# Kernel tuning notes

Measured on AMD Instinct MI355X. Metric: run time of the kernel, lower is better.

## Reference

```python
import jax, jax.numpy as jnp
from jax import lax
import numpy as np

B, S, IN = 8, 4096, 64
D, H, K = 512, 8, 3
TCN_CH = [256, 256, 512]
HD = D // H


def setup_inputs() -> dict:
    key = jax.random.key(0)
    ks = iter(jax.random.split(key, 64))
    def nrm(shape, s=0.02):
        return jax.random.normal(next(ks), shape, jnp.float32) * s
    inp = {"x": jax.random.normal(next(ks), (B, S, IN), jnp.float32)}
    inp["W_in"] = nrm((IN, D)); inp["b_in"] = jnp.zeros((D,), jnp.float32)
    chans = [D] + TCN_CH
    for i in range(3):
        cin, cout = chans[i], chans[i + 1]
        inp[f"c1w{i}"] = nrm((cout, cin, K), 0.01); inp[f"c1b{i}"] = jnp.zeros((cout,), jnp.float32)
        inp[f"c2w{i}"] = nrm((cout, cout, K), 0.01); inp[f"c2b{i}"] = jnp.zeros((cout,), jnp.float32)
        if cin != cout:  # downsample 1x1 conv (blocks 0 and 2)
            inp[f"dsw{i}"] = nrm((cout, cin, 1), 0.01); inp[f"dsb{i}"] = jnp.zeros((cout,), jnp.float32)
    inp["W_tcn"] = nrm((TCN_CH[-1], D)); inp["b_tcn"] = jnp.zeros((D,), jnp.float32)
    NL = 2  # attention layers, stacked on leading axis
    for n in ["Wq", "Wk", "Wv", "Wo"]:
        inp[n] = nrm((NL, D, D))
    for n in ["bq", "bk", "bv", "bo", "ln_b"]:
        inp[n] = jnp.zeros((NL, D), jnp.float32)
    inp["ln_g"] = jnp.ones((NL, D), jnp.float32)
    inp["W_out"] = nrm((D, 1)); inp["b_out"] = jnp.zeros((1,), jnp.float32)
    return inp


def _conv(x, w, b, dil, pad):
    # x: (B,C,L), w: (O,I,K)
    y = lax.conv_general_dilated(x, w, (1,), [(pad, pad)], rhs_dilation=(dil,),
                                 dimension_numbers=("NCH", "OIH", "NCH"))
    return y + b[None, :, None]


def _block(t, c1w, c1b, c2w, c2b, ds, dil):
    # TemporalConvBlock: symmetric padding (k-1)*dil on both convs, truncate to input length
    pad = (K - 1) * dil
    o = jax.nn.relu(_conv(t, c1w, c1b, dil, pad))   # length L + pad
    o = _conv(o, c2w, c2b, dil, pad)                # length L + 2*pad
    r = t if ds is None else _conv(t, ds[0], ds[1], 1, 0)
    return jax.nn.relu(o[:, :, : t.shape[2]] + r)


def _layernorm(x, g, b, eps=1e-5):
    mu = x.mean(-1, keepdims=True)
    var = ((x - mu) ** 2).mean(-1, keepdims=True)
    return (x - mu) * lax.rsqrt(var + eps) * g + b


def _forward(x, W_in, b_in, c1w0, c1b0, c2w0, c2b0, dsw0, dsb0,
             c1w1, c1b1, c2w1, c2b1, c1w2, c1b2, c2w2, c2b2, dsw2, dsb2,
             W_tcn, b_tcn, Wq, bq, Wk, bk, Wv, bv, Wo, bo, ln_g, ln_b, W_out, b_out):
    h = x @ W_in + b_in                              # (B,S,D)
    t = jnp.swapaxes(h, 1, 2)                        # (B,D,S)
    t = _block(t, c1w0, c1b0, c2w0, c2b0, (dsw0, dsb0), 1)
    t = _block(t, c1w1, c1b1, c2w1, c2b1, None, 2)
    t = _block(t, c1w2, c1b2, c2w2, c2b2, (dsw2, dsb2), 4)
    h = h + jnp.swapaxes(t, 1, 2) @ W_tcn + b_tcn
    # sinusoidal positional encoding
    pos = jnp.arange(S, dtype=jnp.float32)[:, None]
    div = jnp.exp(jnp.arange(0, D, 2, dtype=jnp.float32) * (-np.log(10000.0) / D))
    pe = jnp.stack([jnp.sin(pos * div), jnp.cos(pos * div)], axis=-1).reshape(S, D)
    h = h + pe[None]
    for l in range(Wq.shape[0]):
        res = h
        def heads(y):  # (B,S,D) -> (B,H,S,HD)
            return y.reshape(B, S, H, HD).transpose(0, 2, 1, 3)
        q = heads(h @ Wq[l] + bq[l])
        k = heads(h @ Wk[l] + bk[l])
        v = heads(h @ Wv[l] + bv[l])
        qf = jax.nn.elu(q) + 1.0
        kf = jax.nn.elu(k) + 1.0
        kv = jnp.einsum("bhnd,bhnm->bhdm", kf, v)            # (B,H,HD,HD)
        out = jnp.einsum("bhnd,bhdm->bhnm", qf, kv)          # (B,H,S,HD)
        norm = jnp.maximum(jnp.einsum("bhnd,bhd->bhn", qf, kf.sum(2)), 1e-6)
        out = out / norm[..., None]
        out = out.transpose(0, 2, 1, 3).reshape(B, S, D)
        h = _layernorm(res + out @ Wo[l] + bo[l], ln_g[l], ln_b[l])
    pooled = h.mean(1)                                       # (B,D)
    return (pooled @ W_out + b_out)[:, 0]                    # (B,)


def reference(x, W_in, b_in, c1w0, c1b0, c2w0, c2b0, dsw0, dsb0,
              c1w1, c1b1, c2w1, c2b1, c1w2, c1b2, c2w2, c2b2, dsw2, dsb2,
              W_tcn, b_tcn, Wq, bq, Wk, bk, Wv, bv, Wo, bo, ln_g, ln_b, W_out, b_out):
    return _forward(x, W_in, b_in, c1w0, c1b0, c2w0, c2b0, dsw0, dsb0,
                    c1w1, c1b1, c2w1, c2b1, c1w2, c1b2, c2w2, c2b2, dsw2, dsb2,
                    W_tcn, b_tcn, Wq, bq, Wk, bk, Wv, bv, Wo, bo, ln_g, ln_b, W_out, b_out)
```

## Files before the change

### kernel.cpp

```cpp
#include <hip/hip_runtime.h>

typedef unsigned short u16;
typedef unsigned int u32;
typedef short bhalf8 __attribute__((ext_vector_type(8)));
typedef float f32x4 __attribute__((ext_vector_type(4)));

#define S_LEN 4096
#define NSEG 30

__device__ __forceinline__ float b2f(u16 h){ return __uint_as_float(((u32)h) << 16); }
__device__ __forceinline__ u16 f2b(float f){
  u32 u = __float_as_uint(f);
  return (u16)((u + 0x7FFFu + ((u >> 16) & 1u)) >> 16);
}
__device__ __forceinline__ u32 cvtpk(float a, float b){
  u32 r; asm("v_cvt_pk_bf16_f32 %0, %1, %2" : "=v"(r) : "v"(a), "v"(b)); return r;
}
__device__ __forceinline__ void unp8(uint4 v, float* f){
  f[0]=__uint_as_float(v.x<<16); f[1]=__uint_as_float(v.x&0xffff0000u);
  f[2]=__uint_as_float(v.y<<16); f[3]=__uint_as_float(v.y&0xffff0000u);
  f[4]=__uint_as_float(v.z<<16); f[5]=__uint_as_float(v.z&0xffff0000u);
  f[6]=__uint_as_float(v.w<<16); f[7]=__uint_as_float(v.w&0xffff0000u);
}
__device__ __forceinline__ void unp4(uint2 v, float* f){
  f[0]=__uint_as_float(v.x<<16); f[1]=__uint_as_float(v.x&0xffff0000u);
  f[2]=__uint_as_float(v.y<<16); f[3]=__uint_as_float(v.y&0xffff0000u);
}

__device__ __forceinline__ size_t taddr(int r, int c, int C){
  return (size_t)(r >> 7) * ((size_t)C << 7) + (size_t)((c >> 5) << 12)
       + ((r & 127) << 5) + (c & 31);
}

__device__ __forceinline__ void gload16(const void* g, void* l){
  __builtin_amdgcn_global_load_lds(
      (__attribute__((address_space(1))) void*)(g),
      (__attribute__((address_space(3))) void*)(l), 16, 0, 0);
}

struct PrepArgs {
  const float* src[NSEG];
  int N[NSEG]; int K[NSEG]; int sn[NSEG]; int sk[NSEG]; unsigned off[NSEG];
};

__global__ __launch_bounds__(256) void prep_w(PrepArgs pa, u16* __restrict__ wb){
  int seg = blockIdx.y;
  int N = pa.N[seg], K = pa.K[seg];
  int ntk = (K + 31) >> 5;
  int tiles = ((N + 31) >> 5) * ntk;
  int tile = blockIdx.x;
  if (tile >= tiles) return;
  int n0 = (tile / ntk) << 5, k0 = (tile % ntk) << 5;
  const float* src = pa.src[seg];
  long sn = pa.sn[seg], sk = pa.sk[seg];
  u16* dst = wb + pa.off[seg];
  int lk = threadIdx.x & 31, ln = threadIdx.x >> 5;
  #pragma unroll
  for (int i = 0; i < 4; ++i){
    int n = n0 + ln + i*8, k = k0 + lk;
    if (n < N && k < K)
      dst[(size_t)n*K + k] = f2b(src[(long)n*sn + (long)k*sk]);
  }
}

__global__ __launch_bounds__(256) void pe_k(float* __restrict__ pe){
  int id = blockIdx.x*256 + threadIdx.x;
  int s = id >> 8, i = id & 255;
  float div = expf((float)i * (-2.0f * 9.210340371976184f / 512.0f));
  float a = (float)s * div;
  pe[(size_t)s*512 + 2*i]   = sinf(a);
  pe[(size_t)s*512 + 2*i+1] = cosf(a);
}

__global__ __launch_bounds__(256) void cvt_k(const float* __restrict__ x, u16* __restrict__ xb, int n){
  int id = blockIdx.x*256 + threadIdx.x;
  if (id < n){
    int r = id >> 6, c = id & 63;
    xb[taddr(r, c, 64)] = f2b(x[id]);
  }
}

template<int KTOT>
__global__ __launch_bounds__(512, 1) void gemm8_k(
    const u16* __restrict__ A, const u16* __restrict__ W,
    const float* __restrict__ bias, const float* __restrict__ bias2,
    const float* __restrict__ bias3,
    u16* __restrict__ out, const u16* __restrict__ resb,
    const float* __restrict__ peb,
    int N, int nN, int flags)
{
  constexpr int KT = KTOT >> 6;
  constexpr int IT = KT >> 1;
  __shared__ u16 As[2][16384];
  __shared__ u16 Bs[2][16384];
  const int tid = threadIdx.x;
  const int wave = tid >> 6, lane = tid & 63;
  const int wm = wave >> 2, wn = wave & 3;
  const int c0 = lane >> 4, fro = lane & 15;

  const int nwg = gridDim.x;
  const int lin = blockIdx.x;
  const int swz = (lin & 7) * (nwg >> 3) + (lin >> 3);
  const int mb = swz / nN, nb = swz - mb * nN;
  const int m0 = mb << 8, n0 = nb << 8;

  const f32x4 zf = {0.f,0.f,0.f,0.f};
  f32x4 acc[8][4];
  #pragma unroll
  for (int i=0;i<8;++i)
    #pragma unroll
    for (int j=0;j<4;++j) acc[i][j] = zf;

  bhalf8 af[2][2], bf[4][2];

  auto SA = [&](int t, int q){
    int s = (q << 9) + tid;
    int row = s >> 3, phys = s & 7;
    int lc = phys ^ (row & 7);
    int grow = m0 + row;
    int gcol = (t << 6) + (lc << 3);
    size_t ga = ((size_t)(grow >> 7) << 16) + (size_t)((gcol >> 5) << 12)
              + ((grow & 127) << 5) + (gcol & 31);
    gload16(A + ga, &As[t & 1][(q << 12) + (wave << 9)]);
  };
  auto SB = [&](int t, int j){
    int s = (j << 9) + tid;
    int row = s >> 3, phys = s & 7;
    int lc = phys ^ (row & 7);
    gload16(W + (size_t)(n0 + row) * KTOT + (t << 6) + (lc << 3),
            &Bs[t & 1][(j << 12) + (wave << 9)]);
  };
  auto LDB = [&](int t){
    #pragma unroll
    for (int nt=0;nt<4;++nt)
      #pragma unroll
      for (int ks=0;ks<2;++ks){
        int row = (wn << 6) + (nt << 4) + fro;
        int phys = ((ks << 2) + c0) ^ (row & 7);
        bf[nt][ks] = *(const bhalf8*)&Bs[t & 1][(row << 6) + (phys << 3)];
      }
  };
  auto LDA = [&](int t, int q){
    #pragma unroll
    for (int mtl=0;mtl<2;++mtl)
      #pragma unroll
      for (int ks=0;ks<2;++ks){
        int row = (q << 6) + (wm << 5) + (mtl << 4) + fro;
        int phys = ((ks << 2) + c0) ^ (row & 7);
        af[mtl][ks] = *(const bhalf8*)&As[t & 1][(row << 6) + (phys << 3)];
      }
  };
  auto BAR = [&]{
    __builtin_amdgcn_sched_barrier(0);
    __builtin_amdgcn_s_barrier();
    __builtin_amdgcn_sched_barrier(0);
  };
  auto MM = [&](int q){
    __builtin_amdgcn_s_setprio(1);
    #pragma unroll
    for (int mtl=0;mtl<2;++mtl)
      #pragma unroll
      for (int nt=0;nt<4;++nt){
        acc[(q<<1)+mtl][nt] = __builtin_amdgcn_mfma_f32_16x16x32_bf16(
            bf[nt][0], af[mtl][0], acc[(q<<1)+mtl][nt], 0, 0, 0);
        acc[(q<<1)+mtl][nt] = __builtin_amdgcn_mfma_f32_16x16x32_bf16(
            bf[nt][1], af[mtl][1], acc[(q<<1)+mtl][nt], 0, 0, 0);
      }
    __builtin_amdgcn_s_setprio(0);
  };

  #pragma unroll
  for (int x=0;x<4;++x){ SA(0,x); SB(0,x); }
  #pragma unroll
  for (int x=0;x<3;++x){ SA(1,x); SB(1,x); }
  asm volatile("s_waitcnt vmcnt(6)" ::: "memory");
  BAR();

  #pragma unroll
  for (int i=0;i<IT;++i){
    const int t0 = 2*i, t1 = 2*i+1, t2 = 2*i+2, t3 = 2*i+3;
    #pragma unroll
    for (int q=0;q<4;++q){
      if (q == 0) LDB(t0);
      LDA(t0, q);
      if (q == 0){ SA(t1,3); SB(t1,3); }
      else if (t2 < KT){ SA(t2,q-1); SB(t2,q-1); }
      BAR();
      MM(q);
      if (q == 3){
        if (t2 < KT) asm volatile("s_waitcnt vmcnt(6)" ::: "memory");
        else         asm volatile("s_waitcnt vmcnt(0)" ::: "memory");
      }
      BAR();
    }
    #pragma unroll
    for (int q=0;q<4;++q){
      if (q == 0) LDB(t1);
      LDA(t1, q);
      if (q == 0){ if (t2 < KT){ SA(t2,3); SB(t2,3); } }
      else if (t3 < KT){ SA(t3,q-1); SB(t3,q-1); }
      BAR();
      MM(q);
      if (q == 3 && (i + 1 < IT))
        asm volatile("s_waitcnt vmcnt(6)" ::: "memory");
      BAR();
    }
  }

  const int th = n0 >> 9;
  #pragma unroll
  for (int mt = 0; mt < 8; ++mt){
    const int row = m0 + ((mt >> 1) << 6) + (wm << 5) + ((mt & 1) << 4) + fro;
    const size_t prow = (size_t)(row & (S_LEN - 1)) * 512;
    #pragma unroll
    for (int nt = 0; nt < 4; ++nt){
      const int col = n0 + (wn << 6) + (nt << 4) + (c0 << 2);
      float v0 = acc[mt][nt][0], v1 = acc[mt][nt][1], v2 = acc[mt][nt][2], v3 = acc[mt][nt][3];
      if (flags & 32){
        const float* bp = (th == 0) ? bias : ((th == 1) ? bias2 : bias3);
        if (bp){ float4 b4 = *(const float4*)&bp[col & 511]; v0+=b4.x; v1+=b4.y; v2+=b4.z; v3+=b4.w; }
      } else {
        if (bias){ float4 b4 = *(const float4*)&bias[col]; v0+=b4.x; v1+=b4.y; v2+=b4.z; v3+=b4.w; }
      }
      if (flags & 4){
        uint2 rv = *(const uint2*)(resb + taddr(row, col, N));
        float rf[4]; unp4(rv, rf);
        v0 += rf[0]; v1 += rf[1]; v2 += rf[2]; v3 += rf[3];
      }
      if (flags & 8){
        float4 p4 = *(const float4*)&peb[prow + col];
        v0 += p4.x; v1 += p4.y; v2 += p4.z; v3 += p4.w;
      }
      if (flags & 1){
        v0 = fmaxf(v0, 0.f); v1 = fmaxf(v1, 0.f); v2 = fmaxf(v2, 0.f); v3 = fmaxf(v3, 0.f);
      }
      if ((flags & 2) && (!(flags & 32) || th < 2)){
        v0 = (v0 > 0.f) ? (v0 + 1.f) : __expf(v0);
        v1 = (v1 > 0.f) ? (v1 + 1.f) : __expf(v1);
        v2 = (v2 > 0.f) ? (v2 + 1.f) : __expf(v2);
        v3 = (v3 > 0.f) ? (v3 + 1.f) : __expf(v3);
      }
      uint2 pk; pk.x = cvtpk(v0, v1); pk.y = cvtpk(v2, v3);
      *(uint2*)(out + taddr(row, col, N)) = pk;
    }
  }
}

template<int NTAPS, int KS1, int KS2>
__global__ __launch_bounds__(256) void gemm_k(
    const u16* __restrict__ A, const u16* __restrict__ W,
    const u16* __restrict__ A2, const u16* __restrict__ W2,
    const float* __restrict__ bias, const float* __restrict__ bias2,
    const float* __restrict__ bias3,
    u16* __restrict__ out, const u16* __restrict__ resb,
    const float* __restrict__ peb, const float* __restrict__ den,
    int N, int CA, int CA2, int dil, int nN, int wbstride, int flags)
{
  constexpr bool MT   = (NTAPS == 3);
  constexpr int HALO  = MT ? 8 : 0;
  constexpr int AR    = MT ? 144 : 128;
  constexpr int DA    = (!MT) ? 3 : ((KS2 > 0) ? 4 : 2);
  constexpr int DB    = MT ? 4 : 3;
  constexpr int K     = KS1 << 5;
  constexpr int K2    = KS2 << 5;
  constexpr int TOTAL = MT ? (3*KS1 + KS2) : (KS1 + KS2);
  __shared__ u16 As[DA][AR*32];
  __shared__ u16 Bs[DB][128*32];
  const int tid = threadIdx.x;
  const int wave = tid >> 6, lane = tid & 63;
  const int wm = wave >> 1, wn = wave & 1;

  const int nwg = gridDim.x;
  const int lin = blockIdx.x;
  const int swz = (lin & 7) * (nwg >> 3) + (lin >> 3);
  const int mb = swz / nN, nb = swz - mb * nN;
  const int m0 = mb << 7, n0 = nb << 7;
  const bool bnd = (m0 & (S_LEN - 1)) == 0;

  const u16* Ae = (flags & 16) ? (A + (((size_t)(n0 & 511) >> 5) << 12)) : A;

  const int lr4 = lane >> 2, lc4 = lane & 3;
  const int c0 = lane >> 4, fro = lane & 15;

  const f32x4 zf = {0.f, 0.f, 0.f, 0.f};
  const bhalf8 zb = {0,0,0,0,0,0,0,0};
  f32x4 acc[4][4];
  #pragma unroll
  for (int i=0;i<4;++i)
    #pragma unroll
    for (int j=0;j<4;++j) acc[i][j] = zf;

  const u16* Wb = W + (size_t)(m0 >> 12) * (size_t)wbstride;
  const size_t abase  = (size_t)mb * ((size_t)CA  << 7);
  const size_t abase2 = (size_t)mb * ((size_t)CA2 << 7);

  auto STAGE_A = [&](int kb, int ab){
    const size_t tb = abase + ((size_t)kb << 12);
    #pragma unroll
    for (int half = 0; half < 2; ++half){
      int mrow = (wave << 5) + (half << 4) + lr4;
      int i = mrow + HALO;
      int cg = lc4 ^ ((i >> 1) & 3);
      gload16(Ae + tb + mrow*32 + (cg << 3), &As[ab][(HALO + (wave << 5) + (half << 4)) * 32]);
    }
    if (MT && wave == 0 && lane < 32){
      int j = lr4;
      int cg = lc4 ^ ((j >> 1) & 3);
      size_t hb_ = (mb ? abase - ((size_t)CA << 7) : abase) + ((size_t)kb << 12) + (120 + j)*32;
      gload16(Ae + hb_ + (cg << 3), &As[ab][0]);
    }
  };
  auto STAGE_A2 = [&](int t2, int ab){
    const size_t tb = abase2 + ((size_t)t2 << 12);
    #pragma unroll
    for (int half = 0; half < 2; ++half){
      int mrow = (wave << 5) + (half << 4) + lr4;
      int i = mrow + HALO;
      int cg = lc4 ^ ((i >> 1) & 3);
      gload16(A2 + tb + mrow*32 + (cg << 3), &As[ab][(HALO + (wave << 5) + (half << 4)) * 32]);
    }
  };
  auto STAGE_B = [&](const u16* Wt, size_t kstride, int kb, int bb){
    #pragma unroll
    for (int half = 0; half < 2; ++half){
      int i = (wave << 5) + (half << 4) + lr4;
      int cg = lc4 ^ ((i >> 1) & 3);
      gload16(Wt + (size_t)(n0 + i) * kstride + (kb << 5) + (cg << 3),
              &Bs[bb][((wave << 5) + (half << 4)) * 32]);
    }
  };
  auto DO16 = [&](int ab, int bb, int sh, bool mask){
    bhalf8 af[4], bf[4];
    #pragma unroll
    for (int mt = 0; mt < 4; ++mt){
      int r8 = (wm << 6) + (mt << 4) + fro + HALO + sh;
      af[mt] = *(const bhalf8*)&As[ab][r8 * 32 + ((c0 ^ ((r8 >> 1) & 3)) << 3)];
    }
    if (MT && mask && bnd && wm == 0 && fro + sh < 0) af[0] = zb;
    #pragma unroll
    for (int nt = 0; nt < 4; ++nt){
      int rB = (wn << 6) + (nt << 4) + fro;
      bf[nt] = *(const bhalf8*)&Bs[bb][rB * 32 + ((c0 ^ ((rB >> 1) & 3)) << 3)];
    }
    #pragma unroll
    for (int mt = 0; mt < 4; ++mt)
      #pragma unroll
      for (int nt = 0; nt < 4; ++nt)
        acc[mt][nt] = __builtin_amdgcn_mfma_f32_16x16x32_bf16(bf[nt], af[mt], acc[mt][nt], 0, 0, 0);
  };

  if constexpr (!MT){
    auto STG = [&](int s){
      int b = s % 3;
      if (s < KS1){ STAGE_A(s, b); STAGE_B(Wb, (size_t)K, s, b); }
      else if (KS2 > 0){ STAGE_A2(s - KS1, b); STAGE_B(W2, (size_t)K2, s - KS1, b); }
    };
    STG(0);
    if constexpr (TOTAL > 1) STG(1);
    #pragma unroll
    for (int s = 0; s < TOTAL; ++s){
      if (s + 1 >= TOTAL) asm volatile("s_waitcnt vmcnt(0)" ::: "memory");
      else                asm volatile("s_waitcnt vmcnt(4)" ::: "memory");
      __builtin_amdgcn_sched_barrier(0);
      __builtin_amdgcn_s_barrier();
      __builtin_amdgcn_sched_barrier(0);
      if (s + 2 < TOTAL) STG(s + 2);
      DO16(s % 3, s % 3, 0, false);
    }
  } else {
    auto STG = [&](int s){
      if (s < 3*KS1){
        int kb = s / 3, tap = s % 3;
        if (tap == 0) STAGE_A(kb, kb & (DA-1));
        STAGE_B(Wb + (size_t)tap * N * K, (size_t)K, kb, s & 3);
      } else if (KS2 > 0){
        int t2 = s - 3*KS1;
        STAGE_A2(t2, (KS1 + t2) & (DA-1));
        STAGE_B(W2, (size_t)K2, t2, s & 3);
      }
    };
    STG(0);
    if constexpr (TOTAL > 1) STG(1);
    if constexpr (TOTAL > 2) STG(2);
    #pragma unroll
    for (int s = 0; s < TOTAL; ++s){
      if (s + 1 >= TOTAL)      asm volatile("s_waitcnt vmcnt(0)" ::: "memory");
      else if (s + 2 >= TOTAL) asm volatile("s_waitcnt vmcnt(2)" ::: "memory");
      else                     asm volatile("s_waitcnt vmcnt(4)" ::: "memory");
      __builtin_amdgcn_sched_barrier(0);
      __builtin_amdgcn_s_barrier();
      __builtin_amdgcn_sched_barrier(0);
      if (s + 3 < TOTAL) STG(s + 3);
      if (s < 3*KS1) DO16((s/3) & (DA-1), s & 3, ((s%3) - 2) * dil, true);
      else           DO16((KS1 + (s - 3*KS1)) & (DA-1), s & 3, 0, false);
    }
  }

  const int mb_l = (wm << 6) + fro;
  const int cb_l = (wn << 6) + (c0 << 2);
  const int th = n0 >> 9;
  #pragma unroll
  for (int mt = 0; mt < 4; ++mt){
    const int row = m0 + mb_l + (mt << 4);
    const size_t prow = (size_t)(row & (S_LEN - 1)) * 512;
    #pragma unroll
    for (int nt = 0; nt < 4; ++nt){
      const int col = n0 + cb_l + (nt << 4);
      float v0 = acc[mt][nt][0], v1 = acc[mt][nt][1], v2 = acc[mt][nt][2], v3 = acc[mt][nt][3];
      if (flags & 32){
        const float* bp = (th == 0) ? bias : ((th == 1) ? bias2 : bias3);
        if (bp){ float4 b4 = *(const float4*)&bp[col & 511]; v0+=b4.x; v1+=b4.y; v2+=b4.z; v3+=b4.w; }
      } else {
        if (bias) { float4 b4 = *(const float4*)&bias[col];  v0+=b4.x; v1+=b4.y; v2+=b4.z; v3+=b4.w; }
        if (bias2){ float4 b4 = *(const float4*)&bias2[col]; v0+=b4.x; v1+=b4.y; v2+=b4.z; v3+=b4.w; }
      }
      if (flags & 4){
        uint2 rv = *(const uint2*)(resb + taddr(row, col, N));
        float rf[4]; unp4(rv, rf);
        v0 += rf[0]; v1 += rf[1]; v2 += rf[2]; v3 += rf[3];
      }
      if (flags & 8){
        float4 p4 = *(const float4*)&peb[prow + col];
        v0 += p4.x; v1 += p4.y; v2 += p4.z; v3 += p4.w;
      }
      if (flags & 16){
        float d = fmaxf(den[((size_t)row << 3) + (col >> 6)], 1e-6f);
        float rd = 1.0f / d;
        v0 *= rd; v1 *= rd; v2 *= rd; v3 *= rd;
      }
      if (flags & 1){
        v0 = fmaxf(v0, 0.f); v1 = fmaxf(v1, 0.f); v2 = fmaxf(v2, 0.f); v3 = fmaxf(v3, 0.f);
      }
      if ((flags & 2) && (!(flags & 32) || th < 2)){
        v0 = (v0 > 0.f) ? (v0 + 1.f) : __expf(v0);
        v1 = (v1 > 0.f) ? (v1 + 1.f) : __expf(v1);
        v2 = (v2 > 0.f) ? (v2 + 1.f) : __expf(v2);
        v3 = (v3 > 0.f) ? (v3 + 1.f) : __expf(v3);
      }
      uint2 pk; pk.x = cvtpk(v0, v1); pk.y = cvtpk(v2, v3);
      *(uint2*)(out + taddr(row, col, N)) = pk;
    }
  }
}

__global__ __launch_bounds__(256) void kv_partial(
    const u16* __restrict__ qkv,
    float* __restrict__ kvp, float* __restrict__ ksp)
{
  const int bh = blockIdx.x;
  const int b = bh >> 3, h = bh & 7;
  const int ch = blockIdx.y;
  const int t = threadIdx.x;
  __shared__ u16 kfs[16][64];
  __shared__ u16 vs[16][64];
  float acc[4][4] = {{0.f}};
  float ks[4] = {0.f,0.f,0.f,0.f};
  const int d0 = (t >> 4) << 2;
  const int c0 = (t & 15) << 2;
  const int lr = t >> 4, lc = (t & 15) << 2;
  const int rowbase = (b << 12) + (ch << 9);
  const int ck = 512 + (h << 6) + lc;
  const int cv = 1024 + (h << 6) + lc;
  for (int g = 0; g < 32; ++g){
    int r = rowbase + (g << 4) + lr;
    *(uint2*)&kfs[lr][lc] = *(const uint2*)(qkv + taddr(r, ck, 1536));
    *(uint2*)&vs[lr][lc]  = *(const uint2*)(qkv + taddr(r, cv, 1536));
    __syncthreads();
    #pragma unroll
    for (int i = 0; i < 16; ++i){
      float kv4[4], vv4[4];
      unp4(*(const uint2*)&kfs[i][d0], kv4);
      unp4(*(const uint2*)&vs[i][c0], vv4);
      #pragma unroll
      for (int j=0;j<4;++j)
        #pragma unroll
        for (int k2=0;k2<4;++k2) acc[j][k2] += kv4[j]*vv4[k2];
      if ((t & 15) == 0){
        #pragma unroll
        for (int j=0;j<4;++j) ks[j] += kv4[j];
      }
    }
    __syncthreads();
  }
  float* dst = kvp + ((size_t)(bh << 3) + ch) * 4096;
  #pragma unroll
  for (int j=0;j<4;++j)
    #pragma unroll
    for (int k2=0;k2<4;++k2) dst[(d0+j)*64 + (c0+k2)] = acc[j][k2];
  if ((t & 15) == 0){
    float* kd = ksp + ((size_t)(bh << 3) + ch) * 64;
    #pragma unroll
    for (int j=0;j<4;++j) kd[d0+j] = ks[j];
  }
}

__global__ __launch_bounds__(256) void kvred_k(
    const float* __restrict__ kvp, const float* __restrict__ ksp,
    float* __restrict__ kvf, float* __restrict__ ksf)
{
  int bh = blockIdx.x, t = threadIdx.x;
  for (int e = t; e < 4096; e += 256){
    float s = 0.f;
    #pragma unroll
    for (int ch = 0; ch < 8; ++ch) s += kvp[((size_t)(bh<<3)+ch)*4096 + e];
    kvf[(size_t)bh*4096 + e] = s;
  }
  if (t < 64){
    float s = 0.f;
    #pragma unroll
    for (int ch = 0; ch < 8; ++ch) s += ksp[((size_t)(bh<<3)+ch)*64 + t];
    ksf[bh*64 + t] = s;
  }
}

__global__ __launch_bounds__(256) void den_k(const u16* __restrict__ qkv,
    const float* __restrict__ ksf, float* __restrict__ den)
{
  int id = blockIdx.x*256 + threadIdx.x;
  int r = id >> 3, h = id & 7;
  int b = r >> 12;
  const float* ks = ksf + ((b<<3)+h)*64;
  float s = 0.f;
  for (int d = 0; d < 64; d += 8){
    uint4 vq = *(const uint4*)(qkv + taddr(r, (h << 6) + d, 1536));
    float f[8]; unp8(vq, f);
    #pragma unroll
    for (int j=0;j<8;++j) s += f[j]*ks[d+j];
  }
  den[id] = s;
}

__global__ __launch_bounds__(256) void packkv2_k(const float* __restrict__ kvf, u16* __restrict__ wbd){
  int id = blockIdx.x*256 + threadIdx.x;
  int b = id >> 16;
  int n = (id >> 7) & 511, j = id & 127;
  float v = 0.f;
  if ((j >> 6) == ((n >> 6) & 1))
    v = kvf[((size_t)((b<<3)+(n>>6)))*4096 + (j & 63)*64 + (n & 63)];
  wbd[id] = f2b(v);
}

__global__ __launch_bounds__(256) void ln_k(const u16* __restrict__ in,
    const float* __restrict__ g, const float* __restrict__ beta, u16* __restrict__ out)
{
  int wave = threadIdx.x >> 6, lane = threadIdx.x & 63;
  int row = blockIdx.x*4 + wave;
  size_t ad = taddr(row, lane*8, 512);
  uint4 pv = *(const uint4*)(in + ad);
  float f[8]; unp8(pv, f);
  float s = 0.f, ss = 0.f;
  #pragma unroll
  for (int i=0;i<8;++i){ s += f[i]; ss += f[i]*f[i]; }
  for (int m=1;m<64;m<<=1){ s += __shfl_xor(s,m); ss += __shfl_xor(ss,m); }
  float mean = s * (1.f/512.f);
  float var = ss * (1.f/512.f) - mean*mean;
  float rstd = rsqrtf(fmaxf(var, 0.f) + 1e-5f);
  u16 o[8];
  #pragma unroll
  for (int i=0;i<8;++i){
    int c = lane*8 + i;
    o[i] = f2b((f[i]-mean)*rstd*g[c] + beta[c]);
  }
  *(uint4*)(out + ad) = *(uint4*)o;
}

__global__ __launch_bounds__(256) void pool1_k(const u16* __restrict__ hb,
    const float* __restrict__ wout, const float* __restrict__ g,
    const float* __restrict__ beta, float* __restrict__ part)
{
  int b = blockIdx.x >> 6, ch = blockIdx.x & 63;
  int t = threadIdx.x;
  __shared__ float ws[512];
  __shared__ float red[256];
  __shared__ float S2[2];
  float a0 = 0.f, a1 = 0.f;
  for (int i = t; i < 512; i += 256){
    float w = wout[i];
    float gw = w * g[i];
    ws[i] = gw;
    a0 += gw;
    a1 += w * beta[i];
  }
  red[t] = a0; __syncthreads();
  for (int k2=128;k2;k2>>=1){ if (t<k2) red[t]+=red[t+k2]; __syncthreads(); }
  if (!t) S2[0] = red[0];
  __syncthreads();
  red[t] = a1; __syncthreads();
  for (int k2=128;k2;k2>>=1){ if (t<k2) red[t]+=red[t+k2]; __syncthreads(); }
  if (!t) S2[1] = red[0];
  __syncthreads();
  const float Sgw = S2[0], Sbw = S2[1];

  int r = (b << 12) + (ch << 6) + (t >> 2);
  int c0 = (t & 3) << 7;
  float sd = 0.f, s1 = 0.f, s2 = 0.f;
  for (int i = 0; i < 128; i += 8){
    uint4 v = *(const uint4*)(hb + taddr(r, c0 + i, 512));
    float f[8]; unp8(v, f);
    #pragma unroll
    for (int j=0;j<8;++j){ float x = f[j]; sd += x*ws[c0+i+j]; s1 += x; s2 += x*x; }
  }
  sd += __shfl_xor(sd,1); s1 += __shfl_xor(s1,1); s2 += __shfl_xor(s2,1);
  sd += __shfl_xor(sd,2); s1 += __shfl_xor(s1,2); s2 += __shfl_xor(s2,2);
  float mean = s1 * (1.f/512.f);
  float var  = s2 * (1.f/512.f) - mean*mean;
  float rstd = rsqrtf(fmaxf(var, 0.f) + 1e-5f);
  float rowv = rstd * (sd - mean * Sgw) + Sbw;
  red[t] = ((t & 3) == 0) ? rowv : 0.f;
  __syncthreads();
  for (int k2=128;k2;k2>>=1){ if (t<k2) red[t]+=red[t+k2]; __syncthreads(); }
  if (!t) part[blockIdx.x] = red[0];
}

__global__ __launch_bounds__(64) void pool2_k(const float* __restrict__ part,
    const float* __restrict__ bout, float* __restrict__ out)
{
  int b = blockIdx.x, t = threadIdx.x;
  float s = part[(b << 6) + t];
  for (int m=1;m<64;m<<=1) s += __shfl_xor(s,m);
  if (!t) out[b] = s * (1.f/4096.f) + bout[0];
}

extern "C" void kernel_launch(void* const* d_in, const int* in_sizes, int n_in,
                              void* d_out, int out_size, void* d_ws, size_t ws_size,
                              hipStream_t stream)
{
  (void)in_sizes; (void)n_in; (void)out_size; (void)ws_size;
  const float* x    = (const float*)d_in[0];
  const float* W_in = (const float*)d_in[1];
  const float* b_in = (const float*)d_in[2];
  const float* c1w0 = (const float*)d_in[3];
  const float* c1b0 = (const float*)d_in[4];
  const float* c2w0 = (const float*)d_in[5];
  const float* c2b0 = (const float*)d_in[6];
  const float* dsw0 = (const float*)d_in[7];
  const float* dsb0 = (const float*)d_in[8];
  const float* c1w1 = (const float*)d_in[9];
  const float* c1b1 = (const float*)d_in[10];
  const float* c2w1 = (const float*)d_in[11];
  const float* c2b1 = (const float*)d_in[12];
  const float* c1w2 = (const float*)d_in[13];
  const float* c1b2 = (const float*)d_in[14];
  const float* c2w2 = (const float*)d_in[15];
  const float* c2b2 = (const float*)d_in[16];
  const float* dsw2 = (const float*)d_in[17];
  const float* dsb2 = (const float*)d_in[18];
  const float* W_tcn= (const float*)d_in[19];
  const float* b_tcn= (const float*)d_in[20];
  const float* Wq   = (const float*)d_in[21];
  const float* Wk   = (const float*)d_in[22];
  const float* Wv   = (const float*)d_in[23];
  const float* Wo   = (const float*)d_in[24];
  const float* bq   = (const float*)d_in[25];
  const float* bk   = (const float*)d_in[26];
  const float* bv   = (const float*)d_in[27];
  const float* bo   = (const float*)d_in[28];
  const float* lnb  = (const float*)d_in[29];
  const float* lng  = (const float*)d_in[30];
  const float* W_out= (const float*)d_in[31];
  const float* b_out= (const float*)d_in[32];

  char* base = (char*)d_ws;
  size_t off = 0;
  auto alloc = [&](size_t bytes) -> void* {
    void* p = base + off;
    off += (bytes + 255) & ~(size_t)255;
    return p;
  };
  u16* WB   = (u16*)alloc(4816896ull*2);
  u16* wbd  = (u16*)alloc(8ull*512*128*2);
  float* peb= (float*)alloc(4096ull*512*4);
  float* den= (float*)alloc(32768ull*8*4);
  float* kvp= (float*)alloc(512ull*4096*4);
  float* ksp= (float*)alloc(512ull*64*4);
  float* kvf= (float*)alloc(64ull*4096*4);
  float* ksf= (float*)alloc(64ull*64*4);
  float* part=(float*)alloc(512*4);
  u16* hb   = (u16*)alloc(32768ull*512*2);
  char* qkvR= (char*)alloc(32768ull*1536*2);
  u16* atto = (u16*)alloc(32768ull*512*2);

  u16* qkvb = (u16*)qkvR;
  u16* xb   = (u16*)(qkvR);
  u16* t1b  = (u16*)(qkvR + 4194304);
  u16* t2b  = (u16*)(qkvR + 20971520);
  u16* t3b  = (u16*)(qkvR + 37748736);
  u16* o1b  = atto;

  unsigned wo_ = 0;
  auto wseg = [&](unsigned e){ unsigned o = wo_; wo_ += e; return o; };
  unsigned oWin  = wseg(512*64);
  unsigned oC1w0 = wseg(3*256*512);
  unsigned oC2w0 = wseg(3*256*256);
  unsigned oDs0  = wseg(256*512);
  unsigned oC1w1 = wseg(3*256*256);
  unsigned oC2w1 = wseg(3*256*256);
  unsigned oC1w2 = wseg(3*512*256);
  unsigned oC2w2 = wseg(3*512*512);
  unsigned oDs2  = wseg(512*256);
  unsigned oWtcn = wseg(512*512);
  unsigned oQKV  = wseg(2*1536*512);
  unsigned oWo   = wseg(2*512*512);

  PrepArgs pa;
  int si = 0;
  auto seg = [&](const float* s, int N, int K, int sn, int sk, unsigned o){
    pa.src[si]=s; pa.N[si]=N; pa.K[si]=K; pa.sn[si]=sn; pa.sk[si]=sk; pa.off[si]=o; ++si;
  };
  seg(W_in, 512, 64, 1, 512, oWin);
  for (int t=0;t<3;++t) seg(c1w0 + t, 256, 512, 1536, 3, oC1w0 + t*131072);
  for (int t=0;t<3;++t) seg(c2w0 + t, 256, 256,  768, 3, oC2w0 + t*65536);
  seg(dsw0, 256, 512, 512, 1, oDs0);
  for (int t=0;t<3;++t) seg(c1w1 + t, 256, 256,  768, 3, oC1w1 + t*65536);
  for (int t=0;t<3;++t) seg(c2w1 + t, 256, 256,  768, 3, oC2w1 + t*65536);
  for (int t=0;t<3;++t) seg(c1w2 + t, 512, 256,  768, 3, oC1w2 + t*131072);
  for (int t=0;t<3;++t) seg(c2w2 + t, 512, 512, 1536, 3, oC2w2 + t*262144);
  seg(dsw2, 512, 256, 256, 1, oDs2);
  seg(W_tcn, 512, 512, 1, 512, oWtcn);
  for (int l=0;l<2;++l){
    seg(Wq + l*262144, 512, 512, 1, 512, oQKV + l*786432 + 0);
    seg(Wk + l*262144, 512, 512, 1, 512, oQKV + l*786432 + 262144);
    seg(Wv + l*262144, 512, 512, 1, 512, oQKV + l*786432 + 524288);
  }
  for (int l=0;l<2;++l) seg(Wo + l*262144, 512, 512, 1, 512, oWo + l*262144);

  prep_w<<<dim3(256, NSEG), 256, 0, stream>>>(pa, WB);
  pe_k<<<4096, 256, 0, stream>>>(peb);
  cvt_k<<<8192, 256, 0, stream>>>(x, xb, 32768*64);

  const int RELU=1, ELU1=2, RES=4, PE=8, DIV=16, QKV=32;
  auto gemm = [&](const u16* A, const u16* W, const u16* A2, const u16* W2,
                  const float* b1, const float* b2, const float* b3,
                  u16* out, const u16* resb,
                  int K, int K2, int N, int CA, int CA2, int ntaps,
                  int dil, int wbs, int flags){
    int nN = N >> 7;
    dim3 grid(256 * nN);
    if (ntaps == 3){
      if (K == 512 && K2 == 0)
        gemm_k<3,16,0><<<grid, 256, 0, stream>>>(A, W, A2, W2, b1, b2, b3, out, resb,
                                                 peb, den, N, CA, CA2, dil, nN, wbs, flags);
      else if (K == 256 && K2 == 512)
        gemm_k<3,8,16><<<grid, 256, 0, stream>>>(A, W, A2, W2, b1, b2, b3, out, resb,
                                                 peb, den, N, CA, CA2, dil, nN, wbs, flags);
      else if (K == 256 && K2 == 0)
        gemm_k<3,8,0><<<grid, 256, 0, stream>>>(A, W, A2, W2, b1, b2, b3, out, resb,
                                                peb, den, N, CA, CA2, dil, nN, wbs, flags);
      else
        gemm_k<3,16,8><<<grid, 256, 0, stream>>>(A, W, A2, W2, b1, b2, b3, out, resb,
                                                 peb, den, N, CA, CA2, dil, nN, wbs, flags);
    } else {
      if (K == 64)
        gemm_k<1,2,0><<<grid, 256, 0, stream>>>(A, W, A2, W2, b1, b2, b3, out, resb,
                                                peb, den, N, CA, CA2, dil, nN, wbs, flags);
      else
        gemm_k<1,4,0><<<grid, 256, 0, stream>>>(A, W, A2, W2, b1, b2, b3, out, resb,
                                                peb, den, N, CA, CA2, dil, nN, wbs, flags);
    }
  };
  auto gemm8 = [&](const u16* A, const u16* W, const float* b1, const float* b2,
                   const float* b3, u16* out, const u16* resb, int N, int flags){
    int nN = N >> 8;
    gemm8_k<512><<<dim3(128 * nN), 512, 0, stream>>>(A, W, b1, b2, b3, out, resb,
                                                     peb, N, nN, flags);
  };

  gemm(xb, WB + oWin, nullptr, nullptr, b_in, nullptr, nullptr, hb, nullptr,
       64, 0, 512, 64, 0, 1, 1, 0, 0);
  gemm(hb,  WB + oC1w0, nullptr, nullptr, c1b0, nullptr, nullptr, o1b, nullptr,
       512, 0, 256, 512, 0, 3, 1, 0, RELU);
  gemm(o1b, WB + oC2w0, hb, WB + oDs0, c2b0, dsb0, nullptr, t1b, nullptr,
       256, 512, 256, 256, 512, 3, 1, 0, RELU);
  gemm(t1b, WB + oC1w1, nullptr, nullptr, c1b1, nullptr, nullptr, o1b, nullptr,
       256, 0, 256, 256, 0, 3, 2, 0, RELU);
  gemm(o1b, WB + oC2w1, nullptr, nullptr, c2b1, nullptr, nullptr, t2b, t1b,
       256, 0, 256, 256, 0, 3, 2, 0, RELU|RES);
  gemm(t2b, WB + oC1w2, nullptr, nullptr, c1b2, nullptr, nullptr, o1b, nullptr,
       256, 0, 512, 256, 0, 3, 4, 0, RELU);
  gemm(o1b, WB + oC2w2, t2b, WB + oDs2, c2b2, dsb2, nullptr, t3b, nullptr,
       512, 256, 512, 512, 256, 3, 4, 0, RELU);
  gemm8(t3b, WB + oWtcn, b_tcn, nullptr, nullptr, hb, hb, 512, RES|PE);

  for (int l = 0; l < 2; ++l){
    gemm8(hb, WB + oQKV + l*786432, bq + l*512, bk + l*512, bv + l*512,
          qkvb, nullptr, 1536, ELU1|QKV);
    kv_partial<<<dim3(64, 8), 256, 0, stream>>>(qkvb, kvp, ksp);
    kvred_k<<<64, 256, 0, stream>>>(kvp, ksp, kvf, ksf);
    den_k<<<1024, 256, 0, stream>>>(qkvb, ksf, den);
    packkv2_k<<<2048, 256, 0, stream>>>(kvf, wbd);
    gemm(qkvb, wbd, nullptr, nullptr, nullptr, nullptr, nullptr, atto, nullptr,
         128, 0, 512, 1536, 0, 1, 1, 512*128, DIV);
    gemm8(atto, WB + oWo + l*262144, bo + l*512, nullptr, nullptr, hb, hb, 512, RES);
    if (l == 0)
      ln_k<<<8192, 256, 0, stream>>>(hb, lng, lnb, hb);
  }

  pool1_k<<<512, 256, 0, stream>>>(hb, W_out, lng + 512, lnb + 512, part);
  pool2_k<<<8, 64, 0, stream>>>(part, b_out, (float*)d_out);
}
```

Measured before the change: 774.7 us.

## Shrink multi-tap conv GEMM pipeline to depth two and fuse den/pack kernels

The three-tap convolution GEMM path drops from a 4-deep B buffer with 3-stage prefetch to a 3-deep ring with 2-stage prefetch, using modulo indexing and looser vmcnt waits. The smaller LDS footprint may allow more resident workgroups, at the cost of less latency hiding per block. Separately, the denominator kernel and the KV packing kernel become one launch that picks its work by block index, removing one kernel launch per attention layer.

Result: no change. 763.3 us (-1.5%).

```diff
diff --git a/kernel.cpp b/kernel.cpp
--- a/kernel.cpp
+++ b/kernel.cpp
@@ -259,8 +259,8 @@
   constexpr bool MT   = (NTAPS == 3);
   constexpr int HALO  = MT ? 8 : 0;
   constexpr int AR    = MT ? 144 : 128;
-  constexpr int DA    = (!MT) ? 3 : ((KS2 > 0) ? 4 : 2);
-  constexpr int DB    = MT ? 4 : 3;
+  constexpr int DA    = MT ? ((KS2 > 0) ? 3 : 2) : 3;
+  constexpr int DB    = 3;
   constexpr int K     = KS1 << 5;
   constexpr int K2    = KS2 << 5;
   constexpr int TOTAL = MT ? (3*KS1 + KS2) : (KS1 + KS2);
@@ -371,28 +371,26 @@
     auto STG = [&](int s){
       if (s < 3*KS1){
         int kb = s / 3, tap = s % 3;
-        if (tap == 0) STAGE_A(kb, kb & (DA-1));
-        STAGE_B(Wb + (size_t)tap * N * K, (size_t)K, kb, s & 3);
+        if (tap == 0) STAGE_A(kb, kb % DA);
+        STAGE_B(Wb + (size_t)tap * N * K, (size_t)K, kb, s % 3);
       } else if (KS2 > 0){
         int t2 = s - 3*KS1;
-        STAGE_A2(t2, (KS1 + t2) & (DA-1));
-        STAGE_B(W2, (size_t)K2, t2, s & 3);
+        STAGE_A2(t2, (KS1 + t2) % DA);
+        STAGE_B(W2, (size_t)K2, t2, s % 3);
       }
     };
     STG(0);
     if constexpr (TOTAL > 1) STG(1);
-    if constexpr (TOTAL > 2) STG(2);
     #pragma unroll
     for (int s = 0; s < TOTAL; ++s){
-      if (s + 1 >= TOTAL)      asm volatile("s_waitcnt vmcnt(0)" ::: "memory");
-      else if (s + 2 >= TOTAL) asm volatile("s_waitcnt vmcnt(2)" ::: "memory");
-      else                     asm volatile("s_waitcnt vmcnt(4)" ::: "memory");
+      if (s + 1 >= TOTAL) asm volatile("s_waitcnt vmcnt(0)" ::: "memory");
+      else                asm volatile("s_waitcnt vmcnt(2)" ::: "memory");
       __builtin_amdgcn_sched_barrier(0);
       __builtin_amdgcn_s_barrier();
       __builtin_amdgcn_sched_barrier(0);
-      if (s + 3 < TOTAL) STG(s + 3);
-      if (s < 3*KS1) DO16((s/3) & (DA-1), s & 3, ((s%3) - 2) * dil, true);
-      else           DO16((KS1 + (s - 3*KS1)) & (DA-1), s & 3, 0, false);
+      if (s + 2 < TOTAL) STG(s + 2);
+      if (s < 3*KS1) DO16((s/3) % DA, s % 3, ((s%3) - 2) * dil, true);
+      else           DO16((KS1 + (s - 3*KS1)) % DA, s % 3, 0, false);
     }
   }
 
@@ -513,31 +511,33 @@
   }
 }
 
-__global__ __launch_bounds__(256) void den_k(const u16* __restrict__ qkv,
-    const float* __restrict__ ksf, float* __restrict__ den)
-{
-  int id = blockIdx.x*256 + threadIdx.x;
-  int r = id >> 3, h = id & 7;
-  int b = r >> 12;
-  const float* ks = ksf + ((b<<3)+h)*64;
-  float s = 0.f;
-  for (int d = 0; d < 64; d += 8){
-    uint4 vq = *(const uint4*)(qkv + taddr(r, (h << 6) + d, 1536));
-    float f[8]; unp8(vq, f);
-    #pragma unroll
-    for (int j=0;j<8;++j) s += f[j]*ks[d+j];
-  }
-  den[id] = s;
-}
-
-__global__ __launch_bounds__(256) void packkv2_k(const float* __restrict__ kvf, u16* __restrict__ wbd){
-  int id = blockIdx.x*256 + threadIdx.x;
-  int b = id >> 16;
-  int n = (id >> 7) & 511, j = id & 127;
-  float v = 0.f;
-  if ((j >> 6) == ((n >> 6) & 1))
-    v = kvf[((size_t)((b<<3)+(n>>6)))*4096 + (j & 63)*64 + (n & 63)];
-  wbd[id] = f2b(v);
+__global__ __launch_bounds__(256) void denpack_k(const u16* __restrict__ qkv,
+    const float* __restrict__ ksf, float* __restrict__ den,
+    const float* __restrict__ kvf, u16* __restrict__ wbd)
+{
+  int bid = blockIdx.x;
+  if (bid < 1024){
+    int id = bid*256 + threadIdx.x;
+    int r = id >> 3, h = id & 7;
+    int b = r >> 12;
+    const float* ks = ksf + ((b<<3)+h)*64;
+    float s = 0.f;
+    for (int d = 0; d < 64; d += 8){
+      uint4 vq = *(const uint4*)(qkv + taddr(r, (h << 6) + d, 1536));
+      float f[8]; unp8(vq, f);
+      #pragma unroll
+      for (int j=0;j<8;++j) s += f[j]*ks[d+j];
+    }
+    den[id] = s;
+  } else {
+    int id = (bid - 1024)*256 + threadIdx.x;
+    int b = id >> 16;
+    int n = (id >> 7) & 511, j = id & 127;
+    float v = 0.f;
+    if ((j >> 6) == ((n >> 6) & 1))
+      v = kvf[((size_t)((b<<3)+(n>>6)))*4096 + (j & 63)*64 + (n & 63)];
+    wbd[id] = f2b(v);
+  }
 }
 
 __global__ __launch_bounds__(256) void ln_k(const u16* __restrict__ in,
@@ -786,8 +786,7 @@
           qkvb, nullptr, 1536, ELU1|QKV);
     kv_partial<<<dim3(64, 8), 256, 0, stream>>>(qkvb, kvp, ksp);
     kvred_k<<<64, 256, 0, stream>>>(kvp, ksp, kvf, ksf);
-    den_k<<<1024, 256, 0, stream>>>(qkvb, ksf, den);
-    packkv2_k<<<2048, 256, 0, stream>>>(kvf, wbd);
+    denpack_k<<<3072, 256, 0, stream>>>(qkvb, ksf, den, kvf, wbd);
     gemm(qkvb, wbd, nullptr, nullptr, nullptr, nullptr, nullptr, atto, nullptr,
          128, 0, 512, 1536, 0, 1, 1, 512*128, DIV);
     gemm8(atto, WB + oWo + l*262144, bo + l*512, nullptr, nullptr, hb, hb, 512, RES);
```
